# Kernel tuning notes

Measured on AMD Instinct MI355X. Metric: run time of the kernel, lower is better.

## Reference

```python
import jax, jax.numpy as jnp
import numpy as np

N_HEADS, N_MODES, C_IN, C_OUT, SPD = 4, 32, 32, 32, 3


def setup_inputs() -> dict:
    key = jax.random.key(0)
    ks = jax.random.split(key, 9)
    B, NX, NY, NZ = 2, 48, 48, 48
    omega, c = 30.0 / 300.0, 6.0
    a = jax.random.normal(ks[0], (B, NX, NY, NZ, C_IN), jnp.float32)
    x = jax.random.uniform(ks[1], (B, NX, NY, NZ, SPD), jnp.float32)
    y = jax.random.uniform(ks[2], (B, NX, NY, NZ, SPD), jnp.float32)
    a_scale = np.sqrt(c / (C_IN + N_MODES)).astype(np.float32)
    x_scale = (np.sqrt(c / (SPD + N_MODES)) * omega).astype(np.float32)
    u_scale = np.sqrt(c / (N_HEADS * N_MODES + C_OUT)).astype(np.float32)
    a_modes = a_scale * (2 * jax.random.uniform(ks[3], (N_HEADS, N_MODES, C_IN), jnp.float32) - 1)
    x_modes = x_scale * (2 * jax.random.uniform(ks[4], (N_HEADS, N_MODES, SPD), jnp.float32) - 1)
    y_modes = x_scale * (2 * jax.random.uniform(ks[5], (N_HEADS, N_MODES, SPD), jnp.float32) - 1)
    u_modes = u_scale * (2 * jax.random.uniform(ks[6], (N_HEADS, N_MODES, C_OUT), jnp.float32) - 1)
    lim = 1.0 / np.sqrt(C_IN)
    fc_w = jax.random.uniform(ks[7], (C_OUT, C_IN), jnp.float32, -lim, lim)
    fc_b = jax.random.uniform(ks[8], (C_OUT,), jnp.float32, -lim, lim)
    return dict(a=a, x=x, y=y, a_modes=a_modes, x_modes=x_modes,
                y_modes=y_modes, u_modes=u_modes, fc_w=fc_w, fc_b=fc_b)


def _spectral_attention(a, x, y, a_modes, x_modes, y_modes, u_modes):
    # a: (b,nx,ny,nz,i); x,y: (b,nx,ny,nz,d)
    A = jnp.einsum('bxyzi,hfi->bhxyzf', a, a_modes)  # real
    X = jnp.exp(-2j * np.pi * jnp.einsum('bxyzd,hgd->bhxyzg', x, x_modes))
    Y = jnp.exp(2j * np.pi * jnp.einsum('bxyzd,hgd->bhxyzg', y, y_modes))
    n_xyz = y.shape[1] * y.shape[2] * y.shape[3]
    AX = jnp.einsum('bhxyzf,bhxyzg->bhfg', A.astype(X.dtype), X)
    U = jnp.einsum('bhfg,bhxyzg->bhxyzf', AX, Y).real / n_xyz
    return jnp.einsum('bhxyzf,hfo->bxyzo', U, u_modes)


def reference(a, x, y, a_modes, x_modes, y_modes, u_modes, fc_w, fc_b):
    att = _spectral_attention(a, x, y, a_modes, x_modes, y_modes, u_modes)
    skip = jnp.einsum('bxyzi,oi->bxyzo', a, fc_w) + fc_b
    return jax.nn.gelu(att + skip, approximate=False)
```

## Files before the change

kernel.cpp:

```cpp
#include <hip/hip_runtime.h>
#include <hip/hip_bf16.h>
#include <math.h>

#define NHEADS 4
#define NM 32
#define CIN 32
#define COUT 32
#define BATCH 2
#define NPTS (48*48*48)
#define PAD 36
#define PTS_AX 288
#define SEGS_AX (NPTS/PTS_AX)
#define PADT 292
#define SEGS_OUT (NPTS/128)
#define INV_N (1.0f / (float)NPTS)

typedef unsigned short ushort_t;
typedef __attribute__((ext_vector_type(8))) short short8;
typedef __attribute__((ext_vector_type(16))) float floatx16;

#define MFMA32 __builtin_amdgcn_mfma_f32_32x32x16_bf16

union frag8 { short8 v; uint2 u2[2]; unsigned u[4]; ushort_t s[8]; };

__device__ __forceinline__ floatx16 zero16() {
    floatx16 z;
#pragma unroll
    for (int i = 0; i < 16; ++i) z[i] = 0.0f;
    return z;
}
__device__ __forceinline__ ushort_t f2bf(float f) {
    __hip_bfloat16 h = __float2bfloat16(f);
    return *(ushort_t*)&h;
}
__device__ __forceinline__ float bf2f(ushort_t u) {
    union { unsigned i; float f; } v; v.i = ((unsigned)u) << 16; return v.f;
}
__device__ __forceinline__ unsigned pk2(float a, float b) {
    return (unsigned)f2bf(a) | ((unsigned)f2bf(b) << 16);
}
__device__ __forceinline__ short8 frag_lds(const ushort_t* p) {
    frag8 r;
    r.u2[0] = *(const uint2*)p;
    r.u2[1] = *(const uint2*)(p + 4);
    return r.v;
}

__global__ __launch_bounds__(256, 4) void k_ax(
    const float* __restrict__ a, const float* __restrict__ x,
    const float* __restrict__ x_modes,
    float* __restrict__ AX, float* __restrict__ part, int use_part)
{
    __shared__ ushort_t s_aT[CIN][PADT];
    __shared__ float4   s_x4[PTS_AX];

    const int t = threadIdx.x;
    const int w = t >> 6;
    const int l = t & 63;
    const int l31 = l & 31, lh = l >> 5;
    const int b  = blockIdx.x / SEGS_AX;
    const int sb = blockIdx.x % SEGS_AX;
    const int pbase = b * NPTS + sb * PTS_AX;

    for (int pt = t; pt < PTS_AX; pt += 256) {
        const float* arow = a + (size_t)(pbase + pt) * CIN;
#pragma unroll
        for (int v = 0; v < 8; ++v) {
            float4 f = ((const float4*)arow)[v];
            s_aT[4*v+0][pt] = f2bf(f.x);
            s_aT[4*v+1][pt] = f2bf(f.y);
            s_aT[4*v+2][pt] = f2bf(f.z);
            s_aT[4*v+3][pt] = f2bf(f.w);
        }
    }
    for (int idx = t; idx < PTS_AX*3; idx += 256) {
        const float v = x[(size_t)pbase * 3 + idx];
        const int pt = idx / 3;
        ((float*)&s_x4[pt])[idx - 3*pt] = v;
    }
    const float xm0 = x_modes[(w*NM + l31)*3 + 0];
    const float xm1 = x_modes[(w*NM + l31)*3 + 1];
    const float xm2 = x_modes[(w*NM + l31)*3 + 2];

    floatx16 accre = zero16(), accim = zero16();
    __syncthreads();

    for (int c = 0; c < PTS_AX/32; ++c) {
        const int p0 = c * 32;
        short8 xre[2], xim[2];
#pragma unroll
        for (int kh = 0; kh < 2; ++kh) {
            frag8 re_, im_;
#pragma unroll
            for (int j = 0; j < 8; j += 2) {
                const int pl = p0 + kh*16 + lh*8 + j;
                const float4 v0 = s_x4[pl], v1 = s_x4[pl + 1];
                const float q0 = v0.x*xm0 + v0.y*xm1 + v0.z*xm2;
                const float q1 = v1.x*xm0 + v1.y*xm1 + v1.z*xm2;
                re_.u[j>>1] = pk2( __builtin_amdgcn_cosf(q0),  __builtin_amdgcn_cosf(q1));
                im_.u[j>>1] = pk2(-__builtin_amdgcn_sinf(q0), -__builtin_amdgcn_sinf(q1));
            }
            xre[kh] = re_.v; xim[kh] = im_.v;
        }
#pragma unroll
        for (int kh = 0; kh < 2; ++kh) {
            short8 atf = frag_lds(&s_aT[l31][p0 + kh*16 + lh*8]);
            accre = MFMA32(atf, xre[kh], accre, 0, 0, 0);
            accim = MFMA32(atf, xim[kh], accim, 0, 0, 0);
        }
    }

    if (use_part) {
        float* pr = part + (size_t)blockIdx.x * 8192;
#pragma unroll
        for (int r = 0; r < 16; ++r) {
            const int ir = (r & 3) + 8*(r >> 2) + 4*lh;
            const int idx = (w*NM + ir)*NM + l31;
            pr[idx]        = accre[r];
            pr[idx + 4096] = accim[r];
        }
    } else {
        float* Mre = AX;
        float* Mim = AX + BATCH*NHEADS*NM*NM;
#pragma unroll
        for (int r = 0; r < 16; ++r) {
            const int ir = (r & 3) + 8*(r >> 2) + 4*lh;
            const int idx = b*4096 + (w*NM + ir)*NM + l31;
            atomicAdd(&Mre[idx], accre[r]);
            atomicAdd(&Mim[idx], accim[r]);
        }
    }
}

__global__ void k_red(const float* __restrict__ part, float* __restrict__ AX)
{
    __shared__ float s_red[8][32];
    const int t = threadIdx.x, q = t >> 5, l = t & 31;
    const int o = blockIdx.x * 32 + l;
    const int bb = o >> 13, idx = o & 8191;
    float acc = 0.f;
#pragma unroll 6
    for (int sb = q; sb < SEGS_AX; sb += 8)
        acc += part[((size_t)(bb*SEGS_AX + sb))*8192 + idx];
    s_red[q][l] = acc;
    __syncthreads();
    if (t < 32) {
        float s = 0.f;
#pragma unroll
        for (int qq = 0; qq < 8; ++qq) s += s_red[qq][t];
        const int oo = blockIdx.x * 32 + t;
        const int b2 = oo >> 13, i2 = oo & 8191;
        if (i2 < 4096) AX[b2*4096 + i2] = s;
        else           AX[8192 + b2*4096 + (i2 - 4096)] = s;
    }
}

__global__ void k_w(const float* __restrict__ AX, const float* __restrict__ a_modes,
                    const float* __restrict__ u_modes, ushort_t* __restrict__ W)
{
    __shared__ float sM[2][NM][NM];
    __shared__ float sT[2][NM][NM + 1];
    const int t = threadIdx.x;
    const int b = blockIdx.x >> 2, h = blockIdx.x & 3;
    const float* Mre = AX + b*4096 + h*1024;
    const float* Mim = AX + BATCH*4096 + b*4096 + h*1024;
    for (int i = t; i < 1024; i += 256) {
        sM[0][i >> 5][i & 31] = Mre[i];
        sM[1][i >> 5][i & 31] = Mim[i];
    }
    __syncthreads();
    const int fo = t >> 3;
    const int g0 = (t & 7) * 4;
    {
        const float* am = a_modes + (h*NM + fo)*CIN;
        float tr[4] = {0,0,0,0}, ti[4] = {0,0,0,0};
#pragma unroll 8
        for (int i = 0; i < CIN; ++i) {
            const float wv = am[i];
#pragma unroll
            for (int j = 0; j < 4; ++j) {
                tr[j] += wv * sM[0][i][g0+j];
                ti[j] += wv * sM[1][i][g0+j];
            }
        }
#pragma unroll
        for (int j = 0; j < 4; ++j) { sT[0][fo][g0+j] = tr[j]; sT[1][fo][g0+j] = ti[j]; }
    }
    __syncthreads();
    {
        float wr[4] = {0,0,0,0}, wi[4] = {0,0,0,0};
#pragma unroll 8
        for (int f = 0; f < NM; ++f) {
            const float wv = u_modes[(h*NM + f)*COUT + fo];
#pragma unroll
            for (int j = 0; j < 4; ++j) {
                wr[j] += wv * sT[0][f][g0+j];
                wi[j] += wv * sT[1][f][g0+j];
            }
        }
        ushort_t* Wre = W + (size_t)blockIdx.x * 1024;
        ushort_t* Wim = Wre + 8192;
#pragma unroll
        for (int j = 0; j < 4; ++j) {
            Wre[fo*NM + g0 + j] = f2bf(wr[j] * INV_N);
            Wim[fo*NM + g0 + j] = f2bf(wi[j] * INV_N);
        }
    }
}

__global__ __launch_bounds__(256, 4) void k_out(
    const float* __restrict__ a, const float* __restrict__ y,
    const float* __restrict__ y_modes, const ushort_t* __restrict__ Wg,
    const float* __restrict__ fc_w, const float* __restrict__ fc_b,
    float* __restrict__ out)
{
    __shared__ ushort_t s_Wre[NHEADS][NM][PAD];
    __shared__ ushort_t s_Wim[NHEADS][NM][PAD];
    __shared__ float4   s_ym4[NHEADS][NM];
    __shared__ float4   s_y4[128];
    __shared__ ushort_t s_ah[128][PAD];

    const int t = threadIdx.x, w = t >> 6, l = t & 63;
    const int l31 = l & 31, lh = l >> 5;
    const int b  = blockIdx.x / SEGS_OUT;
    const int sb = blockIdx.x % SEGS_OUT;
    const int pblock = b * NPTS + sb * 128;
    const int pwave  = pblock + w * 32;

    {
        const unsigned* wr = (const unsigned*)Wg + b*2048;
        const unsigned* wi = (const unsigned*)(Wg + 8192) + b*2048;
        for (int idx2 = t; idx2 < 2048; idx2 += 256) {
            const int h = idx2 >> 9, o = (idx2 >> 4) & 31, g2 = (idx2 & 15) * 2;
            *(unsigned*)&s_Wre[h][o][g2] = wr[idx2];
            *(unsigned*)&s_Wim[h][o][g2] = wi[idx2];
        }
    }
    if (t < 128) {
        const int h = t >> 5, g = t & 31;
        const float* p = y_modes + (h*NM + g)*3;
        float4 v; v.x = p[0]; v.y = p[1]; v.z = p[2]; v.w = 0.f;
        s_ym4[h][g] = v;
    }
    for (int idx = t; idx < 128*3; idx += 256) {
        const float v = y[(size_t)pblock * 3 + idx];
        const int pt = idx / 3;
        ((float*)&s_y4[pt])[idx - 3*pt] = v;
    }
    if (t < 128) {
        const float* arow = a + (size_t)(pblock + t) * CIN;
        unsigned* dst = (unsigned*)&s_ah[t][0];
#pragma unroll
        for (int v = 0; v < 8; ++v) {
            float4 f = ((const float4*)arow)[v];
            dst[2*v]   = pk2(f.x, f.y);
            dst[2*v+1] = pk2(f.z, f.w);
        }
    }
    short8 whi[2], wlo[2];
#pragma unroll
    for (int kh = 0; kh < 2; ++kh) {
        const float* p = fc_w + l31*CIN + kh*16 + lh*8;
        float4 f0 = ((const float4*)p)[0], f1 = ((const float4*)p)[1];
        float v[8] = {f0.x,f0.y,f0.z,f0.w,f1.x,f1.y,f1.z,f1.w};
        frag8 hi, lo;
#pragma unroll
        for (int j = 0; j < 8; ++j) {
            const ushort_t hb = f2bf(v[j]);
            hi.s[j] = hb;
            lo.s[j] = f2bf(v[j] - bf2f(hb));
        }
        whi[kh] = hi.v; wlo[kh] = lo.v;
    }
    const float fb = fc_b[l31];

    __syncthreads();
    const float4 y3 = s_y4[w*32 + l31];

    floatx16 acc = zero16();
#pragma unroll
    for (int kh = 0; kh < 2; ++kh) {
        short8 af = frag_lds(&s_ah[w*32 + l31][kh*16 + lh*8]);
        acc = MFMA32(af, whi[kh], acc, 0, 0, 0);
        acc = MFMA32(af, wlo[kh], acc, 0, 0, 0);
    }
    for (int h = 0; h < NHEADS; ++h) {
        short8 yre[2], yim[2];
#pragma unroll
        for (int kh = 0; kh < 2; ++kh) {
            frag8 re_, im_;
#pragma unroll
            for (int j = 0; j < 8; j += 2) {
                const int g0 = kh*16 + lh*8 + j;
                const float4 m0 = s_ym4[h][g0], m1 = s_ym4[h][g0 + 1];
                const float p0 = y3.x*m0.x + y3.y*m0.y + y3.z*m0.z;
                const float p1 = y3.x*m1.x + y3.y*m1.y + y3.z*m1.z;
                re_.u[j>>1] = pk2( __builtin_amdgcn_cosf(p0),  __builtin_amdgcn_cosf(p1));
                im_.u[j>>1] = pk2(-__builtin_amdgcn_sinf(p0), -__builtin_amdgcn_sinf(p1));
            }
            yre[kh] = re_.v; yim[kh] = im_.v;
        }
#pragma unroll
        for (int kh = 0; kh < 2; ++kh) {
            short8 wrf = frag_lds(&s_Wre[h][l31][kh*16 + lh*8]);
            short8 wif = frag_lds(&s_Wim[h][l31][kh*16 + lh*8]);
            acc = MFMA32(yre[kh], wrf, acc, 0, 0, 0);
            acc = MFMA32(yim[kh], wif, acc, 0, 0, 0);
        }
    }
#pragma unroll
    for (int r = 0; r < 16; ++r) {
        const int ptr_ = (r & 3) + 8*(r >> 2) + 4*lh;
        const float z = acc[r] + fb;
        out[(size_t)(pwave + ptr_) * COUT + l31] =
            0.5f * z * (1.0f + erff(z * 0.70710678118654752f));
    }
}

extern "C" void kernel_launch(void* const* d_in, const int* in_sizes, int n_in,
                              void* d_out, int out_size, void* d_ws, size_t ws_size,
                              hipStream_t stream) {
    (void)in_sizes; (void)n_in; (void)out_size;
    const float* a       = (const float*)d_in[0];
    const float* x       = (const float*)d_in[1];
    const float* y       = (const float*)d_in[2];
    const float* a_modes = (const float*)d_in[3];
    const float* x_modes = (const float*)d_in[4];
    const float* y_modes = (const float*)d_in[5];
    const float* u_modes = (const float*)d_in[6];
    const float* fc_w    = (const float*)d_in[7];
    const float* fc_b    = (const float*)d_in[8];
    float* out  = (float*)d_out;
    float*    AX   = (float*)d_ws;
    ushort_t* W    = (ushort_t*)((char*)d_ws + 65536);
    float*    part = (float*)((char*)d_ws + 98304);

    const size_t need = 98304 + (size_t)BATCH * SEGS_AX * 8192 * sizeof(float);
    const int use_part = (ws_size >= need) ? 1 : 0;

    if (!use_part) hipMemsetAsync(AX, 0, 65536, stream);
    k_ax<<<BATCH * SEGS_AX, 256, 0, stream>>>(a, x, x_modes, AX, part, use_part);
    if (use_part) k_red<<<512, 256, 0, stream>>>(part, AX);
    k_w<<<8, 256, 0, stream>>>(AX, a_modes, u_modes, W);
    k_out<<<BATCH * SEGS_OUT, 256, 0, stream>>>(a, y, y_modes, W, fc_w, fc_b, out);
}
```

Baseline: 150.3 us.

## Fuse partial reduction and W computation via last-block atomic counter

```diff
diff --git a/kernel.cpp b/kernel.cpp
--- a/kernel.cpp
+++ b/kernel.cpp
@@ -13,6 +13,7 @@
 #define SEGS_AX (NPTS/PTS_AX)
 #define PADT 292
 #define SEGS_OUT (NPTS/128)
+#define NRED 512
 #define INV_N (1.0f / (float)NPTS)
 
 typedef unsigned short ushort_t;
@@ -49,7 +50,8 @@
 __global__ __launch_bounds__(256, 4) void k_ax(
     const float* __restrict__ a, const float* __restrict__ x,
     const float* __restrict__ x_modes,
-    float* __restrict__ AX, float* __restrict__ part, int use_part)
+    float* __restrict__ AX, float* __restrict__ part,
+    unsigned* __restrict__ cnt, int use_part)
 {
     __shared__ ushort_t s_aT[CIN][PADT];
     __shared__ float4   s_x4[PTS_AX];
@@ -61,6 +63,9 @@
     const int b  = blockIdx.x / SEGS_AX;
     const int sb = blockIdx.x % SEGS_AX;
     const int pbase = b * NPTS + sb * PTS_AX;
+
+    if (blockIdx.x == 0 && t == 0)
+        __hip_atomic_store(cnt, 0u, __ATOMIC_RELAXED, __HIP_MEMORY_SCOPE_AGENT);
 
     for (int pt = t; pt < PTS_AX; pt += 256) {
         const float* arow = a + (size_t)(pbase + pt) * CIN;
@@ -132,31 +137,120 @@
     }
 }
 
-__global__ void k_red(const float* __restrict__ part, float* __restrict__ AX)
+__global__ void k_redw(const float* __restrict__ part,
+                       const float* __restrict__ a_modes,
+                       const float* __restrict__ u_modes,
+                       float* __restrict__ AX, ushort_t* __restrict__ W,
+                       unsigned* __restrict__ cnt)
 {
-    __shared__ float s_red[8][32];
-    const int t = threadIdx.x, q = t >> 5, l = t & 31;
-    const int o = blockIdx.x * 32 + l;
-    const int bb = o >> 13, idx = o & 8191;
-    float acc = 0.f;
-#pragma unroll 6
-    for (int sb = q; sb < SEGS_AX; sb += 8)
-        acc += part[((size_t)(bb*SEGS_AX + sb))*8192 + idx];
-    s_red[q][l] = acc;
-    __syncthreads();
-    if (t < 32) {
-        float s = 0.f;
-#pragma unroll
-        for (int qq = 0; qq < 8; ++qq) s += s_red[qq][t];
-        const int oo = blockIdx.x * 32 + t;
-        const int b2 = oo >> 13, i2 = oo & 8191;
-        if (i2 < 4096) AX[b2*4096 + i2] = s;
-        else           AX[8192 + b2*4096 + (i2 - 4096)] = s;
-    }
-}
-
-__global__ void k_w(const float* __restrict__ AX, const float* __restrict__ a_modes,
-                    const float* __restrict__ u_modes, ushort_t* __restrict__ W)
+    __shared__ float4   s_r[32][8];
+    __shared__ float    sAm[4][32][32];
+    __shared__ float    sUm[4][32][32];
+    __shared__ float    sP[4][32][33];
+    __shared__ unsigned s_last;
+
+    const int t = threadIdx.x;
+    const int blk = blockIdx.x;
+    const int bb = blk >> 8;
+    const int idx0 = (blk & 255) * 32;
+    const int c = t & 7, s = t >> 3;
+
+    {
+        const float4* p4 = (const float4*)part;
+        const size_t colbase = (size_t)bb * SEGS_AX * 2048 + (idx0 >> 2) + c;
+        float4 acc = {0.f, 0.f, 0.f, 0.f};
+#pragma unroll 4
+        for (int k = 0; k < 12; ++k) {
+            const float4 v = p4[colbase + (size_t)(s + 32*k) * 2048];
+            acc.x += v.x; acc.y += v.y; acc.z += v.z; acc.w += v.w;
+        }
+        s_r[s][c] = acc;
+    }
+    __syncthreads();
+    if (t < 8) {
+        float4 v = s_r[0][t];
+#pragma unroll
+        for (int ss = 1; ss < 32; ++ss) {
+            const float4 u = s_r[ss][t];
+            v.x += u.x; v.y += u.y; v.z += u.z; v.w += u.w;
+        }
+        float* dst = (idx0 < 4096) ? (AX + bb*4096 + idx0)
+                                   : (AX + 8192 + bb*4096 + (idx0 - 4096));
+        ((float4*)dst)[t] = v;
+    }
+    __syncthreads();
+    if (t == 0) {
+        __threadfence();
+        const unsigned prev = __hip_atomic_fetch_add(
+            cnt, 1u, __ATOMIC_ACQ_REL, __HIP_MEMORY_SCOPE_AGENT);
+        s_last = (prev == (unsigned)(NRED - 1)) ? 1u : 0u;
+    }
+    __syncthreads();
+    if (!s_last) return;
+    __threadfence();
+
+    {
+        const float4* am4 = (const float4*)a_modes;
+        const float4* um4 = (const float4*)u_modes;
+        float4* sa4 = (float4*)&sAm[0][0][0];
+        float4* su4 = (float4*)&sUm[0][0][0];
+        for (int e = t; e < 1024; e += 256) { sa4[e] = am4[e]; su4[e] = um4[e]; }
+    }
+    __syncthreads();
+#pragma unroll
+    for (int k = 0; k < 16; ++k) {
+        const int e = k*256 + t;
+        const int h = e >> 10, o = (e >> 5) & 31, i = e & 31;
+        float p = 0.f;
+#pragma unroll
+        for (int f = 0; f < 32; ++f)
+            p += sUm[h][f][o] * sAm[h][f][i];
+        sP[h][o][i] = p;
+    }
+    __syncthreads();
+
+    {
+        const int grp = t >> 3;
+        const int g0 = (t & 7) * 4;
+        const int b = grp >> 4, h = (grp >> 2) & 3, oq = grp & 3;
+        const float* Mre = AX + b*4096 + h*1024;
+        const float* Mim = AX + 8192 + b*4096 + h*1024;
+        float4 ar[8], ai[8];
+#pragma unroll
+        for (int o8 = 0; o8 < 8; ++o8) {
+            ar[o8] = {0.f,0.f,0.f,0.f}; ai[o8] = {0.f,0.f,0.f,0.f};
+        }
+#pragma unroll 4
+        for (int i = 0; i < 32; ++i) {
+            const float4 mr = *(const float4*)&Mre[i*32 + g0];
+            const float4 mi = *(const float4*)&Mim[i*32 + g0];
+#pragma unroll
+            for (int o8 = 0; o8 < 8; ++o8) {
+                const float p = sP[h][oq*8 + o8][i];
+                ar[o8].x += p*mr.x; ar[o8].y += p*mr.y;
+                ar[o8].z += p*mr.z; ar[o8].w += p*mr.w;
+                ai[o8].x += p*mi.x; ai[o8].y += p*mi.y;
+                ai[o8].z += p*mi.z; ai[o8].w += p*mi.w;
+            }
+        }
+        ushort_t* Wre = W + (size_t)(b*4 + h) * 1024;
+        ushort_t* Wim = Wre + 8192;
+#pragma unroll
+        for (int o8 = 0; o8 < 8; ++o8) {
+            const int o = oq*8 + o8;
+            uint2 pr, pi;
+            pr.x = pk2(ar[o8].x*INV_N, ar[o8].y*INV_N);
+            pr.y = pk2(ar[o8].z*INV_N, ar[o8].w*INV_N);
+            pi.x = pk2(ai[o8].x*INV_N, ai[o8].y*INV_N);
+            pi.y = pk2(ai[o8].z*INV_N, ai[o8].w*INV_N);
+            *(uint2*)&Wre[o*32 + g0] = pr;
+            *(uint2*)&Wim[o*32 + g0] = pi;
+        }
+    }
+}
+
+__global__ void k_w_fb(const float* __restrict__ AX, const float* __restrict__ a_modes,
+                       const float* __restrict__ u_modes, ushort_t* __restrict__ W)
 {
     __shared__ float sM[2][NM][NM];
     __shared__ float sT[2][NM][NM + 1];
@@ -333,14 +427,15 @@
     float* out  = (float*)d_out;
     float*    AX   = (float*)d_ws;
     ushort_t* W    = (ushort_t*)((char*)d_ws + 65536);
-    float*    part = (float*)((char*)d_ws + 98304);
-
-    const size_t need = 98304 + (size_t)BATCH * SEGS_AX * 8192 * sizeof(float);
+    unsigned* cnt  = (unsigned*)((char*)d_ws + 98304);
+    float*    part = (float*)((char*)d_ws + 99328);
+
+    const size_t need = 99328 + (size_t)BATCH * SEGS_AX * 8192 * sizeof(float);
     const int use_part = (ws_size >= need) ? 1 : 0;
 
     if (!use_part) hipMemsetAsync(AX, 0, 65536, stream);
-    k_ax<<<BATCH * SEGS_AX, 256, 0, stream>>>(a, x, x_modes, AX, part, use_part);
-    if (use_part) k_red<<<512, 256, 0, stream>>>(part, AX);
-    k_w<<<8, 256, 0, stream>>>(AX, a_modes, u_modes, W);
+    k_ax<<<BATCH * SEGS_AX, 256, 0, stream>>>(a, x, x_modes, AX, part, cnt, use_part);
+    if (use_part) k_redw<<<NRED, 256, 0, stream>>>(part, a_modes, u_modes, AX, W, cnt);
+    else          k_w_fb<<<8, 256, 0, stream>>>(AX, a_modes, u_modes, W);
     k_out<<<BATCH * SEGS_OUT, 256, 0, stream>>>(a, y, y_modes, W, fc_w, fc_b, out);
 }
```

New measurement: 173.6 us. 15.5% more time.
